# Kernel optimization log

Hardware: AMD Instinct MI355X
Metric: run time of the kernel (lower is better)

## Reference

```python
import jax, jax.numpy as jnp
import numpy as np

V_DIM, Q_DIM, NUM_HID = 2048, 1024, 1024
B, K, N = 64, 12, 36


def setup_inputs() -> dict:
    key = jax.random.key(0)
    ks = jax.random.split(key, 8)
    v = jax.random.normal(ks[0], (B, K, N, V_DIM), dtype=jnp.float32)
    q = jax.random.normal(ks[1], (B, K, Q_DIM), dtype=jnp.float32)
    # FCNet layer: weight_norm(Linear(v_dim+q_dim, num_hid), dim=None) + ReLU
    W1 = jax.random.normal(ks[2], (NUM_HID, V_DIM + Q_DIM), dtype=jnp.float32) * 0.02
    g1 = jnp.asarray(1.0, dtype=jnp.float32)  # weight_norm gain (scalar, dim=None)
    b1 = jnp.zeros((NUM_HID,), dtype=jnp.float32)
    # final: weight_norm(Linear(num_hid, 1), dim=None)
    W2 = jax.random.normal(ks[3], (1, NUM_HID), dtype=jnp.float32) * 0.02
    g2 = jnp.asarray(1.0, dtype=jnp.float32)
    b2 = jnp.zeros((1,), dtype=jnp.float32)
    return {"v": v, "q": q, "W1": W1, "g1": g1, "b1": b1, "W2": W2, "g2": g2, "b2": b2}


def reference(v, q, W1, g1, b1, W2, g2, b2):
    # weight_norm with dim=None: W_eff = g * W / ||W||_F (g is a scalar)
    W1e = g1 * W1 / jnp.linalg.norm(W1)   # [num_hid, v_dim+q_dim]
    W2e = g2 * W2 / jnp.linalg.norm(W2)   # [1, num_hid]
    # Avoid materializing the repeated+concatenated [B,K,N,v_dim+q_dim] tensor:
    # cat(v, broadcast(q)) @ W1e^T == v @ W1v^T + q @ W1q^T (q term broadcast over N)
    W1v = W1e[:, :V_DIM]                  # [num_hid, v_dim]
    W1q = W1e[:, V_DIM:]                  # [num_hid, q_dim]
    hv = jnp.einsum('bknv,hv->bknh', v, W1v)          # [B,K,N,num_hid]
    hq = jnp.einsum('bkq,hq->bkh', q, W1q)            # [B,K,num_hid]
    joint = jax.nn.relu(hv + hq[:, :, None, :] + b1)  # FCNet: weight-norm Linear + ReLU
    logits = jnp.einsum('bknh,oh->bkno', joint, W2e) + b2  # [B,K,N,1]
    w = jax.nn.softmax(logits, axis=1)                # softmax over k (dim 1)
    return w
```

## Files before the change

kernel.cpp:

```cpp
#include <hip/hip_runtime.h>

#define V_DIM   2048
#define Q_DIM   1024
#define NUM_HID 1024
#define BB 64
#define KK 12
#define NN 36
#define M_ROWS (BB*KK*NN)
#define BKROWS (BB*KK)

typedef unsigned short u16;
typedef __bf16 bf16x8  __attribute__((ext_vector_type(8)));
typedef u16    ushort8 __attribute__((ext_vector_type(8)));
typedef float  floatx4 __attribute__((ext_vector_type(4)));

__device__ __forceinline__ u16 f2bf(float f) {
    unsigned u = __float_as_uint(f);
    u += 0x7fffu + ((u >> 16) & 1u);
    return (u16)(u >> 16);
}

__device__ __forceinline__ void gload16(const u16* g, u16* l) {
    __builtin_amdgcn_global_load_lds((const __attribute__((address_space(1))) void*)g,
                                     (__attribute__((address_space(3))) void*)l, 16, 0, 0);
}

__global__ void norm_w1_kernel(const float* __restrict__ W1, float* __restrict__ acc)
{
    float s = 0.f;
    const float4* p = (const float4*)W1;
    const int total = (NUM_HID * (V_DIM + Q_DIM)) / 4;
    for (int i = blockIdx.x * 256 + threadIdx.x; i < total; i += 256 * 256) {
        float4 f = p[i];
        s += f.x * f.x + f.y * f.y + f.z * f.z + f.w * f.w;
    }
    #pragma unroll
    for (int off = 32; off > 0; off >>= 1) s += __shfl_down(s, off);
    __shared__ float red[4];
    if ((threadIdx.x & 63) == 0) red[threadIdx.x >> 6] = s;
    __syncthreads();
    if (threadIdx.x == 0) atomicAdd(acc, red[0] + red[1] + red[2] + red[3]);
}

__global__ void scale_kernel(const float* __restrict__ W2, const float* __restrict__ g1,
                             const float* __restrict__ g2, float* __restrict__ wsf)
{
    float v = W2[threadIdx.x];
    float s = v * v;
    #pragma unroll
    for (int off = 32; off > 0; off >>= 1) s += __shfl_down(s, off);
    __shared__ float red[16];
    if ((threadIdx.x & 63) == 0) red[threadIdx.x >> 6] = s;
    __syncthreads();
    if (threadIdx.x == 0) {
        float t = 0.f;
        #pragma unroll
        for (int u = 0; u < 16; u++) t += red[u];
        wsf[2] = g1[0] / sqrtf(wsf[0]);
        wsf[3] = g2[0] / sqrtf(t);
    }
}

__global__ void convert_w1_kernel(const float* __restrict__ W1,
                                  u16* __restrict__ W1v, u16* __restrict__ W1q)
{
    int s = blockIdx.x * 256 + threadIdx.x;
    if (s >= NUM_HID * (V_DIM + Q_DIM) / 8) return;
    int h = s / 384, g = s % 384;
    const float4* p = (const float4*)(W1 + (size_t)h * (V_DIM + Q_DIM) + g * 8);
    float4 a = p[0], b = p[1];
    ushort8 o;
    o[0]=f2bf(a.x); o[1]=f2bf(a.y); o[2]=f2bf(a.z); o[3]=f2bf(a.w);
    o[4]=f2bf(b.x); o[5]=f2bf(b.y); o[6]=f2bf(b.z); o[7]=f2bf(b.w);
    if (g < 256) *(ushort8*)(W1v + (size_t)h * V_DIM + g * 8) = o;
    else         *(ushort8*)(W1q + (size_t)h * Q_DIM + (g - 256) * 8) = o;
}

__global__ void convert_v_kernel(const float* __restrict__ v, u16* __restrict__ vbf)
{
    const int total = (M_ROWS * V_DIM) / 8;
    for (int s = blockIdx.x * 256 + threadIdx.x; s < total; s += 2048 * 256) {
        const float4* p = (const float4*)(v + (size_t)s * 8);
        float4 a = p[0], b = p[1];
        ushort8 o;
        o[0]=f2bf(a.x); o[1]=f2bf(a.y); o[2]=f2bf(a.z); o[3]=f2bf(a.w);
        o[4]=f2bf(b.x); o[5]=f2bf(b.y); o[6]=f2bf(b.z); o[7]=f2bf(b.w);
        *(ushort8*)(vbf + (size_t)s * 8) = o;
    }
}

template<int GK, bool MAIN, bool ABF16>
__global__ __launch_bounds__(256, 2)
void gemm_kernel(const void* __restrict__ Asrc,
                 const u16*  __restrict__ Bsrc,
                 float*      __restrict__ outp,
                 const float* __restrict__ hq,
                 const float* __restrict__ b1,
                 const float* __restrict__ W2,
                 const float* __restrict__ scl)
{
    __shared__ u16 As[ABF16 ? 128 * 64 : 128 * 72];
    __shared__ u16 Bs[128 * 64];

    const int tid  = threadIdx.x;
    const int lane = tid & 63;
    const int wv   = tid >> 6;
    const int wm   = wv & 1;
    const int wn   = wv >> 1;
    const int quad = lane >> 4;
    const int l15  = lane & 15;

    const int bid  = blockIdx.y * 8 + blockIdx.x;
    const int nwg  = gridDim.x * gridDim.y;
    const int tile = (bid & 7) * (nwg >> 3) + (bid >> 3);
    const int tx   = tile & 7;
    const int ty   = tile >> 3;
    const int m0   = ty * 128;
    const int n0   = tx * 128;

    floatx4 acc[4][4];
    #pragma unroll
    for (int i = 0; i < 4; i++)
        #pragma unroll
        for (int j = 0; j < 4; j++)
            acc[i][j] = (floatx4){0.f, 0.f, 0.f, 0.f};

    for (int kt = 0; kt < GK / 64; ++kt) {
        const int k0 = kt * 64;
        __syncthreads();
        if constexpr (ABF16) {
            const u16* Ab = (const u16*)Asrc;
            #pragma unroll
            for (int it = 0; it < 4; ++it) {
                int sbase = it * 256 + wv * 64;
                int s = sbase + lane;
                int r = s >> 3, g = s & 7;
                int gs = g ^ (r & 7);
                gload16(Ab + (size_t)(m0 + r) * GK + k0 + gs * 8, &As[sbase * 8]);
            }
        } else {
            const float* Af = (const float*)Asrc;
            #pragma unroll
            for (int it = 0; it < 4; ++it) {
                int s = tid + 256 * it;
                int r = s >> 3, g = s & 7;
                const float4* gp = (const float4*)(Af + (size_t)(m0 + r) * GK + k0 + g * 8);
                float4 f0 = gp[0];
                float4 f1 = gp[1];
                ushort8 o;
                o[0]=f2bf(f0.x); o[1]=f2bf(f0.y); o[2]=f2bf(f0.z); o[3]=f2bf(f0.w);
                o[4]=f2bf(f1.x); o[5]=f2bf(f1.y); o[6]=f2bf(f1.z); o[7]=f2bf(f1.w);
                *(ushort8*)(&As[r * 72 + g * 8]) = o;
            }
        }
        #pragma unroll
        for (int it = 0; it < 4; ++it) {
            int sbase = it * 256 + wv * 64;
            int s = sbase + lane;
            int c = s >> 3, g = s & 7;
            int gs = g ^ (c & 7);
            gload16(Bsrc + (size_t)(n0 + c) * GK + k0 + gs * 8, &Bs[sbase * 8]);
        }
        __syncthreads();
        #pragma unroll
        for (int ks = 0; ks < 2; ++ks) {
            bf16x8 af[4], bfr[4];
            #pragma unroll
            for (int i = 0; i < 4; i++) {
                int rA = wm * 64 + i * 16 + l15;
                if constexpr (ABF16) {
                    int off = (ks * 32 + quad * 8) ^ ((rA & 7) << 3);
                    af[i] = *(const bf16x8*)(&As[rA * 64 + off]);
                } else {
                    af[i] = *(const bf16x8*)(&As[rA * 72 + ks * 32 + quad * 8]);
                }
            }
            #pragma unroll
            for (int j = 0; j < 4; j++) {
                int c = wn * 64 + j * 16 + l15;
                int off = (ks * 32 + quad * 8) ^ ((c & 7) << 3);
                bfr[j] = *(const bf16x8*)(&Bs[c * 64 + off]);
            }
            #pragma unroll
            for (int i = 0; i < 4; i++)
                #pragma unroll
                for (int j = 0; j < 4; j++)
                    acc[i][j] = __builtin_amdgcn_mfma_f32_16x16x32_bf16(af[i], bfr[j], acc[i][j], 0, 0, 0);
        }
    }

    if constexpr (MAIN) {
        const float s1 = scl[2];
        int   cg[4];
        float w2v[4], b1v[4];
        #pragma unroll
        for (int j = 0; j < 4; j++) {
            cg[j]  = n0 + wn * 64 + j * 16 + l15;
            w2v[j] = W2[cg[j]];
            b1v[j] = b1[cg[j]];
        }
        #pragma unroll
        for (int i = 0; i < 4; i++) {
            #pragma unroll
            for (int r = 0; r < 4; r++) {
                const int mg = m0 + wm * 64 + i * 16 + quad * 4 + r;
                const int bk = mg / NN;
                float p = 0.f;
                #pragma unroll
                for (int j = 0; j < 4; j++) {
                    float pre = s1 * (acc[i][j][r] + hq[(size_t)bk * NUM_HID + cg[j]]) + b1v[j];
                    p += fmaxf(pre, 0.f) * w2v[j];
                }
                p += __shfl_xor(p, 1);
                p += __shfl_xor(p, 2);
                p += __shfl_xor(p, 4);
                p += __shfl_xor(p, 8);
                if (l15 == 0)
                    outp[(size_t)mg * 16 + tx * 2 + wn] = p;
            }
        }
    } else {
        #pragma unroll
        for (int i = 0; i < 4; i++)
            #pragma unroll
            for (int r = 0; r < 4; r++) {
                const int mg = m0 + wm * 64 + i * 16 + quad * 4 + r;
                #pragma unroll
                for (int j = 0; j < 4; j++) {
                    const int c = n0 + wn * 64 + j * 16 + l15;
                    outp[(size_t)mg * NUM_HID + c] = acc[i][j][r];
                }
            }
    }
}

__global__ void softmax_kernel(const float* __restrict__ part,
                               const float* __restrict__ scl,
                               const float* __restrict__ b2,
                               float* __restrict__ out)
{
    int t = blockIdx.x * 256 + threadIdx.x;
    if (t >= BB * NN) return;
    int b = t / NN, n = t % NN;
    float s2 = scl[3], bias = b2[0];
    float lg[KK];
    float mx = -1e30f;
    #pragma unroll
    for (int k = 0; k < KK; k++) {
        int m = (b * KK + k) * NN + n;
        const float4* pp = (const float4*)(part + (size_t)m * 16);
        float4 a0 = pp[0], a1 = pp[1], a2 = pp[2], a3 = pp[3];
        float s = (a0.x + a0.y + a0.z + a0.w) + (a1.x + a1.y + a1.z + a1.w)
                + (a2.x + a2.y + a2.z + a2.w) + (a3.x + a3.y + a3.z + a3.w);
        lg[k] = s2 * s + bias;
        mx = fmaxf(mx, lg[k]);
    }
    float den = 0.f;
    #pragma unroll
    for (int k = 0; k < KK; k++) { lg[k] = expf(lg[k] - mx); den += lg[k]; }
    float inv = 1.0f / den;
    #pragma unroll
    for (int k = 0; k < KK; k++) out[(size_t)((b * KK + k) * NN + n)] = lg[k] * inv;
}

extern "C" void kernel_launch(void* const* d_in, const int* in_sizes, int n_in,
                              void* d_out, int out_size, void* d_ws, size_t ws_size,
                              hipStream_t stream)
{
    (void)in_sizes; (void)n_in; (void)out_size;
    const float* v  = (const float*)d_in[0];
    const float* q  = (const float*)d_in[1];
    const float* W1 = (const float*)d_in[2];
    const float* g1 = (const float*)d_in[3];
    const float* b1 = (const float*)d_in[4];
    const float* W2 = (const float*)d_in[5];
    const float* g2 = (const float*)d_in[6];
    const float* b2 = (const float*)d_in[7];
    float* out = (float*)d_out;

    char*  ws   = (char*)d_ws;
    float* wsf  = (float*)ws;
    float* hq   = (float*)(ws + 16);
    u16*   W1v  = (u16*)  (ws + 16 + 3145728);
    u16*   W1q  = (u16*)  (ws + 16 + 3145728 + 4194304);
    float* part = (float*)(ws + 16 + 3145728 + 4194304 + 2097152);
    u16*   vbf  = (u16*)  (ws + 16 + 3145728 + 4194304 + 2097152 + 1769472);
    const size_t ws_need = 16ull + 3145728 + 4194304 + 2097152 + 1769472
                         + (size_t)M_ROWS * V_DIM * 2;
    const bool pre = (ws_size >= ws_need);

    hipMemsetAsync(d_ws, 0, 16, stream);
    norm_w1_kernel<<<256, 256, 0, stream>>>(W1, wsf);
    scale_kernel<<<1, 1024, 0, stream>>>(W2, g1, g2, wsf);
    convert_w1_kernel<<<1536, 256, 0, stream>>>(W1, W1v, W1q);
    gemm_kernel<Q_DIM, false, false><<<dim3(8, 6), 256, 0, stream>>>(
        q, W1q, hq, nullptr, nullptr, nullptr, wsf);
    if (pre) {
        convert_v_kernel<<<2048, 256, 0, stream>>>(v, vbf);
        gemm_kernel<V_DIM, true, true><<<dim3(8, 216), 256, 0, stream>>>(
            vbf, W1v, part, hq, b1, W2, wsf);
    } else {
        gemm_kernel<V_DIM, true, false><<<dim3(8, 216), 256, 0, stream>>>(
            v, W1v, part, hq, b1, W2, wsf);
    }
    softmax_kernel<<<9, 256, 0, stream>>>(part, wsf, b2, out);
}
```

Before: 556.5 us.

## Add 256x256-tile 8-wave bf16 MFMA GEMM with interleaved LDS staging

Replaces the main v·W1v GEMM on the pre-converted path with a new kernel that uses 512 threads, 256x256 output tiles, double-buffered swizzled LDS and direct global-to-LDS loads. Loads are split into quarter-stages interleaved with four MFMA phases, with raised wave priority around the math and explicit waitcnt/barriers. The grid is remapped for L2 locality and the fused ReLU/W2 epilogue writes 16 partials per row. Larger tiles raise arithmetic intensity and cut global traffic, at the cost of heavy LDS use (128KB) and register pressure that limit occupancy.

```diff
diff --git a/kernel.cpp b/kernel.cpp
--- a/kernel.cpp
+++ b/kernel.cpp
@@ -23,6 +23,16 @@
 __device__ __forceinline__ void gload16(const u16* g, u16* l) {
     __builtin_amdgcn_global_load_lds((const __attribute__((address_space(1))) void*)g,
                                      (__attribute__((address_space(3))) void*)l, 16, 0, 0);
+}
+
+__device__ __forceinline__ void barrier_() {
+    asm volatile("" ::: "memory");
+    __builtin_amdgcn_s_barrier();
+    asm volatile("" ::: "memory");
+}
+__device__ __forceinline__ void lgkm0_() {
+    asm volatile("s_waitcnt lgkmcnt(0)" ::: "memory");
+    __builtin_amdgcn_sched_barrier(0);
 }
 
 __global__ void norm_w1_kernel(const float* __restrict__ W1, float* __restrict__ acc)
@@ -234,6 +244,174 @@
     }
 }
 
+__global__ __launch_bounds__(512, 2)
+void gemm8_kernel(const u16* __restrict__ Asrc, const u16* __restrict__ Bsrc,
+                  float* __restrict__ outp, const float* __restrict__ hq,
+                  const float* __restrict__ b1, const float* __restrict__ W2,
+                  const float* __restrict__ scl)
+{
+    __shared__ u16 As[2][256 * 64];
+    __shared__ u16 Bs[2][256 * 64];
+
+    const int tid  = threadIdx.x;
+    const int lane = tid & 63;
+    const int wv   = tid >> 6;
+    const int wm   = wv >> 2;
+    const int wn   = wv & 3;
+    const int quad = lane >> 4;
+    const int l15  = lane & 15;
+    const int swz  = l15 & 7;
+
+    const int bid  = blockIdx.x;
+    const int tile = (bid & 7) * (gridDim.x >> 3) + (bid >> 3);
+    const int tx   = tile & 3;
+    const int ty   = tile >> 2;
+    const int m0   = ty * 256;
+    const int n0   = tx * 256;
+
+    const int rg   = tid >> 3;
+    const int gsw  = (tid & 7) ^ (rg & 7);
+
+    auto stage = [&](int p, int isB, int half, int t) {
+        const u16* src = isB ? Bsrc : Asrc;
+        const int  b0  = isB ? n0 : m0;
+        u16* dst = isB ? Bs[p] : As[p];
+        #pragma unroll
+        for (int ii = 0; ii < 2; ++ii) {
+            const int row = half * 128 + ii * 64 + rg;
+            u16* d = dst + (size_t)(half * 128 + ii * 64 + wv * 8) * 64;
+            gload16(src + (size_t)(b0 + row) * 2048 + t * 64 + gsw * 8, d);
+        }
+    };
+    auto rdA = [&](int p, int i, int ks) {
+        const int row = wm * 128 + i * 16 + l15;
+        return *(const bf16x8*)(&As[p][row * 64 + (((ks * 4 + quad) ^ swz) * 8)]);
+    };
+    auto rdB = [&](int p, int j, int ks) {
+        const int col = wn * 64 + j * 16 + l15;
+        return *(const bf16x8*)(&Bs[p][col * 64 + (((ks * 4 + quad) ^ swz) * 8)]);
+    };
+
+    floatx4 acc[8][4];
+    #pragma unroll
+    for (int i = 0; i < 8; i++)
+        #pragma unroll
+        for (int j = 0; j < 4; j++)
+            acc[i][j] = (floatx4){0.f, 0.f, 0.f, 0.f};
+
+    bf16x8 aLo[4][2], aHi[4][2], b01[2][2], b23[2][2];
+
+    stage(0, 1, 0, 0);
+    stage(0, 0, 0, 0);
+    stage(0, 0, 1, 0);
+    stage(0, 1, 1, 0);
+    stage(1, 1, 0, 1);
+    stage(1, 0, 0, 1);
+    asm volatile("s_waitcnt vmcnt(4)" ::: "memory");
+    barrier_();
+
+    for (int t = 0; t < 32; ++t) {
+        const int p  = t & 1;
+        const int pn = p ^ 1;
+        const int t1 = (t + 1 < 32) ? t + 1 : 30;
+        const int t2 = (t + 2 < 32) ? t + 2 : 30;
+
+        #pragma unroll
+        for (int i = 0; i < 4; i++) { aLo[i][0] = rdA(p, i, 0); aLo[i][1] = rdA(p, i, 1); }
+        #pragma unroll
+        for (int j = 0; j < 2; j++) { b01[j][0] = rdB(p, j, 0); b01[j][1] = rdB(p, j, 1); }
+        stage(pn, 0, 1, t1);
+        barrier_();
+        lgkm0_();
+        __builtin_amdgcn_s_setprio(1);
+        #pragma unroll
+        for (int i = 0; i < 4; i++)
+            #pragma unroll
+            for (int j = 0; j < 2; j++) {
+                acc[i][j] = __builtin_amdgcn_mfma_f32_16x16x32_bf16(aLo[i][0], b01[j][0], acc[i][j], 0, 0, 0);
+                acc[i][j] = __builtin_amdgcn_mfma_f32_16x16x32_bf16(aLo[i][1], b01[j][1], acc[i][j], 0, 0, 0);
+            }
+        __builtin_amdgcn_s_setprio(0);
+        barrier_();
+
+        #pragma unroll
+        for (int j = 0; j < 2; j++) { b23[j][0] = rdB(p, 2 + j, 0); b23[j][1] = rdB(p, 2 + j, 1); }
+        stage(pn, 1, 1, t1);
+        barrier_();
+        lgkm0_();
+        __builtin_amdgcn_s_setprio(1);
+        #pragma unroll
+        for (int i = 0; i < 4; i++)
+            #pragma unroll
+            for (int j = 0; j < 2; j++) {
+                acc[i][2 + j] = __builtin_amdgcn_mfma_f32_16x16x32_bf16(aLo[i][0], b23[j][0], acc[i][2 + j], 0, 0, 0);
+                acc[i][2 + j] = __builtin_amdgcn_mfma_f32_16x16x32_bf16(aLo[i][1], b23[j][1], acc[i][2 + j], 0, 0, 0);
+            }
+        __builtin_amdgcn_s_setprio(0);
+        barrier_();
+
+        #pragma unroll
+        for (int i = 0; i < 4; i++) { aHi[i][0] = rdA(p, 4 + i, 0); aHi[i][1] = rdA(p, 4 + i, 1); }
+        stage(p, 1, 0, t2);
+        barrier_();
+        lgkm0_();
+        __builtin_amdgcn_s_setprio(1);
+        #pragma unroll
+        for (int i = 0; i < 4; i++)
+            #pragma unroll
+            for (int j = 0; j < 2; j++) {
+                acc[4 + i][j] = __builtin_amdgcn_mfma_f32_16x16x32_bf16(aHi[i][0], b01[j][0], acc[4 + i][j], 0, 0, 0);
+                acc[4 + i][j] = __builtin_amdgcn_mfma_f32_16x16x32_bf16(aHi[i][1], b01[j][1], acc[4 + i][j], 0, 0, 0);
+            }
+        __builtin_amdgcn_s_setprio(0);
+        barrier_();
+
+        stage(p, 0, 0, t2);
+        asm volatile("s_waitcnt vmcnt(4)" ::: "memory");
+        barrier_();
+        __builtin_amdgcn_s_setprio(1);
+        #pragma unroll
+        for (int i = 0; i < 4; i++)
+            #pragma unroll
+            for (int j = 0; j < 2; j++) {
+                acc[4 + i][2 + j] = __builtin_amdgcn_mfma_f32_16x16x32_bf16(aHi[i][0], b23[j][0], acc[4 + i][2 + j], 0, 0, 0);
+                acc[4 + i][2 + j] = __builtin_amdgcn_mfma_f32_16x16x32_bf16(aHi[i][1], b23[j][1], acc[4 + i][2 + j], 0, 0, 0);
+            }
+        __builtin_amdgcn_s_setprio(0);
+        barrier_();
+    }
+
+    const float s1 = scl[2];
+    int   cg[4];
+    float w2v[4], b1v[4];
+    #pragma unroll
+    for (int j = 0; j < 4; j++) {
+        cg[j]  = n0 + wn * 64 + j * 16 + l15;
+        w2v[j] = W2[cg[j]];
+        b1v[j] = b1[cg[j]];
+    }
+    #pragma unroll
+    for (int i = 0; i < 8; i++) {
+        #pragma unroll
+        for (int r = 0; r < 4; r++) {
+            const int mg = m0 + wm * 128 + i * 16 + quad * 4 + r;
+            const int bk = mg / NN;
+            float pv = 0.f;
+            #pragma unroll
+            for (int j = 0; j < 4; j++) {
+                float pre = s1 * (acc[i][j][r] + hq[(size_t)bk * NUM_HID + cg[j]]) + b1v[j];
+                pv += fmaxf(pre, 0.f) * w2v[j];
+            }
+            pv += __shfl_xor(pv, 1);
+            pv += __shfl_xor(pv, 2);
+            pv += __shfl_xor(pv, 4);
+            pv += __shfl_xor(pv, 8);
+            if (l15 == 0)
+                outp[(size_t)mg * 16 + tx * 4 + wn] = pv;
+        }
+    }
+}
+
 __global__ void softmax_kernel(const float* __restrict__ part,
                                const float* __restrict__ scl,
                                const float* __restrict__ b2,
@@ -297,8 +475,7 @@
         q, W1q, hq, nullptr, nullptr, nullptr, wsf);
     if (pre) {
         convert_v_kernel<<<2048, 256, 0, stream>>>(v, vbf);
-        gemm_kernel<V_DIM, true, true><<<dim3(8, 216), 256, 0, stream>>>(
-            vbf, W1v, part, hq, b1, W2, wsf);
+        gemm8_kernel<<<432, 512, 0, stream>>>(vbf, W1v, part, hq, b1, W2, wsf);
     } else {
         gemm_kernel<V_DIM, true, false><<<dim3(8, 216), 256, 0, stream>>>(
             v, W1v, part, hq, b1, W2, wsf);
```

Measured after the change: 565.2 us. Within noise of the previous version (+1.6%).

## Fuse v bf16 conversion into GEMM and merge W1 norm with conversion

Applied to the files above, without the earlier changes.

Removes the standalone pass that converted v to bf16 in workspace; the main GEMM now loads fp32 v and converts it while staging into LDS, using the packed hardware bf16 convert instruction. The W1 Frobenius-norm reduction is folded into the W1 conversion kernel, and softmax uses smaller blocks. This cuts a full read/write of the large activation tensor and two launches, at the cost of a register-staged A load instead of direct global-to-LDS loads.

```diff
diff --git a/kernel.cpp b/kernel.cpp
--- a/kernel.cpp
+++ b/kernel.cpp
@@ -14,10 +14,10 @@
 typedef u16    ushort8 __attribute__((ext_vector_type(8)));
 typedef float  floatx4 __attribute__((ext_vector_type(4)));
 
-__device__ __forceinline__ u16 f2bf(float f) {
-    unsigned u = __float_as_uint(f);
-    u += 0x7fffu + ((u >> 16) & 1u);
-    return (u16)(u >> 16);
+__device__ __forceinline__ unsigned cvtpk(float lo, float hi) {
+    unsigned r;
+    asm("v_cvt_pk_bf16_f32 %0, %1, %2" : "=v"(r) : "v"(lo), "v"(hi));
+    return r;
 }
 
 __device__ __forceinline__ void gload16(const u16* g, u16* l) {
@@ -25,19 +25,25 @@
                                      (__attribute__((address_space(3))) void*)l, 16, 0, 0);
 }
 
-__global__ void norm_w1_kernel(const float* __restrict__ W1, float* __restrict__ acc)
-{
-    float s = 0.f;
-    const float4* p = (const float4*)W1;
-    const int total = (NUM_HID * (V_DIM + Q_DIM)) / 4;
-    for (int i = blockIdx.x * 256 + threadIdx.x; i < total; i += 256 * 256) {
-        float4 f = p[i];
-        s += f.x * f.x + f.y * f.y + f.z * f.z + f.w * f.w;
-    }
-    #pragma unroll
-    for (int off = 32; off > 0; off >>= 1) s += __shfl_down(s, off);
+__global__ void convert_w1_kernel(const float* __restrict__ W1,
+                                  u16* __restrict__ W1v, u16* __restrict__ W1q,
+                                  float* __restrict__ acc)
+{
+    int s = blockIdx.x * 256 + threadIdx.x;
+    int h = s / 384, g = s % 384;
+    const float4* p = (const float4*)(W1 + (size_t)h * (V_DIM + Q_DIM) + g * 8);
+    float4 a = p[0], b = p[1];
+    float ss = a.x*a.x + a.y*a.y + a.z*a.z + a.w*a.w
+             + b.x*b.x + b.y*b.y + b.z*b.z + b.w*b.w;
+    unsigned d0 = cvtpk(a.x, a.y), d1 = cvtpk(a.z, a.w);
+    unsigned d2 = cvtpk(b.x, b.y), d3 = cvtpk(b.z, b.w);
+    uint4 o = make_uint4(d0, d1, d2, d3);
+    if (g < 256) *(uint4*)(W1v + (size_t)h * V_DIM + g * 8) = o;
+    else         *(uint4*)(W1q + (size_t)h * Q_DIM + (g - 256) * 8) = o;
+    #pragma unroll
+    for (int off = 32; off > 0; off >>= 1) ss += __shfl_down(ss, off);
     __shared__ float red[4];
-    if ((threadIdx.x & 63) == 0) red[threadIdx.x >> 6] = s;
+    if ((threadIdx.x & 63) == 0) red[threadIdx.x >> 6] = ss;
     __syncthreads();
     if (threadIdx.x == 0) atomicAdd(acc, red[0] + red[1] + red[2] + red[3]);
 }
@@ -61,45 +67,17 @@
     }
 }
 
-__global__ void convert_w1_kernel(const float* __restrict__ W1,
-                                  u16* __restrict__ W1v, u16* __restrict__ W1q)
-{
-    int s = blockIdx.x * 256 + threadIdx.x;
-    if (s >= NUM_HID * (V_DIM + Q_DIM) / 8) return;
-    int h = s / 384, g = s % 384;
-    const float4* p = (const float4*)(W1 + (size_t)h * (V_DIM + Q_DIM) + g * 8);
-    float4 a = p[0], b = p[1];
-    ushort8 o;
-    o[0]=f2bf(a.x); o[1]=f2bf(a.y); o[2]=f2bf(a.z); o[3]=f2bf(a.w);
-    o[4]=f2bf(b.x); o[5]=f2bf(b.y); o[6]=f2bf(b.z); o[7]=f2bf(b.w);
-    if (g < 256) *(ushort8*)(W1v + (size_t)h * V_DIM + g * 8) = o;
-    else         *(ushort8*)(W1q + (size_t)h * Q_DIM + (g - 256) * 8) = o;
-}
-
-__global__ void convert_v_kernel(const float* __restrict__ v, u16* __restrict__ vbf)
-{
-    const int total = (M_ROWS * V_DIM) / 8;
-    for (int s = blockIdx.x * 256 + threadIdx.x; s < total; s += 2048 * 256) {
-        const float4* p = (const float4*)(v + (size_t)s * 8);
-        float4 a = p[0], b = p[1];
-        ushort8 o;
-        o[0]=f2bf(a.x); o[1]=f2bf(a.y); o[2]=f2bf(a.z); o[3]=f2bf(a.w);
-        o[4]=f2bf(b.x); o[5]=f2bf(b.y); o[6]=f2bf(b.z); o[7]=f2bf(b.w);
-        *(ushort8*)(vbf + (size_t)s * 8) = o;
-    }
-}
-
-template<int GK, bool MAIN, bool ABF16>
+template<int GK, bool MAIN>
 __global__ __launch_bounds__(256, 2)
-void gemm_kernel(const void* __restrict__ Asrc,
-                 const u16*  __restrict__ Bsrc,
-                 float*      __restrict__ outp,
+void gemm_kernel(const float* __restrict__ Asrc,
+                 const u16*   __restrict__ Bsrc,
+                 float*       __restrict__ outp,
                  const float* __restrict__ hq,
                  const float* __restrict__ b1,
                  const float* __restrict__ W2,
                  const float* __restrict__ scl)
 {
-    __shared__ u16 As[ABF16 ? 128 * 64 : 128 * 72];
+    __shared__ u16 As[128 * 72];
     __shared__ u16 Bs[128 * 64];
 
     const int tid  = threadIdx.x;
@@ -128,30 +106,16 @@
     for (int kt = 0; kt < GK / 64; ++kt) {
         const int k0 = kt * 64;
         __syncthreads();
-        if constexpr (ABF16) {
-            const u16* Ab = (const u16*)Asrc;
-            #pragma unroll
-            for (int it = 0; it < 4; ++it) {
-                int sbase = it * 256 + wv * 64;
-                int s = sbase + lane;
-                int r = s >> 3, g = s & 7;
-                int gs = g ^ (r & 7);
-                gload16(Ab + (size_t)(m0 + r) * GK + k0 + gs * 8, &As[sbase * 8]);
-            }
-        } else {
-            const float* Af = (const float*)Asrc;
-            #pragma unroll
-            for (int it = 0; it < 4; ++it) {
-                int s = tid + 256 * it;
-                int r = s >> 3, g = s & 7;
-                const float4* gp = (const float4*)(Af + (size_t)(m0 + r) * GK + k0 + g * 8);
-                float4 f0 = gp[0];
-                float4 f1 = gp[1];
-                ushort8 o;
-                o[0]=f2bf(f0.x); o[1]=f2bf(f0.y); o[2]=f2bf(f0.z); o[3]=f2bf(f0.w);
-                o[4]=f2bf(f1.x); o[5]=f2bf(f1.y); o[6]=f2bf(f1.z); o[7]=f2bf(f1.w);
-                *(ushort8*)(&As[r * 72 + g * 8]) = o;
-            }
+        #pragma unroll
+        for (int it = 0; it < 4; ++it) {
+            int s = tid + 256 * it;
+            int r = s >> 3, g = s & 7;
+            const float4* gp = (const float4*)(Asrc + (size_t)(m0 + r) * GK + k0 + g * 8);
+            float4 f0 = gp[0];
+            float4 f1 = gp[1];
+            unsigned d0 = cvtpk(f0.x, f0.y), d1 = cvtpk(f0.z, f0.w);
+            unsigned d2 = cvtpk(f1.x, f1.y), d3 = cvtpk(f1.z, f1.w);
+            *(uint4*)(&As[r * 72 + g * 8]) = make_uint4(d0, d1, d2, d3);
         }
         #pragma unroll
         for (int it = 0; it < 4; ++it) {
@@ -168,12 +132,7 @@
             #pragma unroll
             for (int i = 0; i < 4; i++) {
                 int rA = wm * 64 + i * 16 + l15;
-                if constexpr (ABF16) {
-                    int off = (ks * 32 + quad * 8) ^ ((rA & 7) << 3);
-                    af[i] = *(const bf16x8*)(&As[rA * 64 + off]);
-                } else {
-                    af[i] = *(const bf16x8*)(&As[rA * 72 + ks * 32 + quad * 8]);
-                }
+                af[i] = *(const bf16x8*)(&As[rA * 72 + ks * 32 + quad * 8]);
             }
             #pragma unroll
             for (int j = 0; j < 4; j++) {
@@ -239,8 +198,7 @@
                                const float* __restrict__ b2,
                                float* __restrict__ out)
 {
-    int t = blockIdx.x * 256 + threadIdx.x;
-    if (t >= BB * NN) return;
+    int t = blockIdx.x * 64 + threadIdx.x;
     int b = t / NN, n = t % NN;
     float s2 = scl[3], bias = b2[0];
     float lg[KK];
@@ -267,7 +225,7 @@
                               void* d_out, int out_size, void* d_ws, size_t ws_size,
                               hipStream_t stream)
 {
-    (void)in_sizes; (void)n_in; (void)out_size;
+    (void)in_sizes; (void)n_in; (void)out_size; (void)ws_size;
     const float* v  = (const float*)d_in[0];
     const float* q  = (const float*)d_in[1];
     const float* W1 = (const float*)d_in[2];
@@ -284,24 +242,13 @@
     u16*   W1v  = (u16*)  (ws + 16 + 3145728);
     u16*   W1q  = (u16*)  (ws + 16 + 3145728 + 4194304);
     float* part = (float*)(ws + 16 + 3145728 + 4194304 + 2097152);
-    u16*   vbf  = (u16*)  (ws + 16 + 3145728 + 4194304 + 2097152 + 1769472);
-    const size_t ws_need = 16ull + 3145728 + 4194304 + 2097152 + 1769472
-                         + (size_t)M_ROWS * V_DIM * 2;
-    const bool pre = (ws_size >= ws_need);
 
     hipMemsetAsync(d_ws, 0, 16, stream);
-    norm_w1_kernel<<<256, 256, 0, stream>>>(W1, wsf);
+    convert_w1_kernel<<<1536, 256, 0, stream>>>(W1, W1v, W1q, wsf);
     scale_kernel<<<1, 1024, 0, stream>>>(W2, g1, g2, wsf);
-    convert_w1_kernel<<<1536, 256, 0, stream>>>(W1, W1v, W1q);
-    gemm_kernel<Q_DIM, false, false><<<dim3(8, 6), 256, 0, stream>>>(
+    gemm_kernel<Q_DIM, false><<<dim3(8, 6), 256, 0, stream>>>(
         q, W1q, hq, nullptr, nullptr, nullptr, wsf);
-    if (pre) {
-        convert_v_kernel<<<2048, 256, 0, stream>>>(v, vbf);
-        gemm_kernel<V_DIM, true, true><<<dim3(8, 216), 256, 0, stream>>>(
-            vbf, W1v, part, hq, b1, W2, wsf);
-    } else {
-        gemm_kernel<V_DIM, true, false><<<dim3(8, 216), 256, 0, stream>>>(
-            v, W1v, part, hq, b1, W2, wsf);
-    }
-    softmax_kernel<<<9, 256, 0, stream>>>(part, wsf, b2, out);
-}
+    gemm_kernel<V_DIM, true><<<dim3(8, 216), 256, 0, stream>>>(
+        v, W1v, part, hq, b1, W2, wsf);
+    softmax_kernel<<<36, 64, 0, stream>>>(part, wsf, b2, out);
+}
```

Result: faster. 537.7 us (-3.4%).
